# Performance work log

Hardware: AMD Instinct MI355X
Metric: run time of the kernel (lower is better)

## Reference

```python
import jax, jax.numpy as jnp
import numpy as np

# NOTE on reconstructed deps (not shown in source):
#  - utils.mmnorm(x): max-magnitude norm, x / (max|x| over last dim + eps)
#  - model.LearnableFourierResampler(din, dout, nf): x -> Linear(din,nf) -> [sin,cos] -> Linear(2nf,dout)
#  - utils.pscan(q, fn, identity): Hillis-Steele log-depth scan: for n in 1,2,4,...:
#        q = fn(x=q, y=shift_right(q, n, fill=identity))   (Scanner.forward(x, y) cats (y, x))

B, T, C, NF = 8, 2048, 1024, 64
EPS = 1e-6

def mmnorm(x):
    return x / (jnp.max(jnp.abs(x), axis=-1, keepdims=True) + EPS)

def setup_inputs() -> dict:
    key = jax.random.key(0)
    ks = jax.random.split(key, 8)
    def w(k, shape, fan_in):
        return jax.random.normal(k, shape, jnp.float32) * (1.0 / np.sqrt(fan_in))
    return {
        "x": jax.random.normal(ks[0], (B, T, C), jnp.float32),
        "attn_W": w(ks[1], (C, 2 * C), C),
        "attn_b": jnp.zeros((2 * C,), jnp.float32),
        "freq_W": w(ks[2], (2 * C, NF), 2 * C),
        "freq_b": jnp.zeros((NF,), jnp.float32),
        "out_W": w(ks[3], (2 * NF, C), 2 * NF),
        "out_b": jnp.zeros((C,), jnp.float32),
        "proj_W": w(ks[4], (C, C), C),
        "proj_b": jnp.zeros((C,), jnp.float32),
        "identity": jax.random.uniform(ks[5], (C,), jnp.float32),
    }

def _scanner(y, x, freq_W, freq_b, out_W, out_b):
    # Scanner.forward(x, y): z = cat((y, x)); Fourier resample; mmnorm
    z = jnp.concatenate([y, x], axis=-1)                      # [B,T,2C]
    f = z @ freq_W + freq_b                                   # [B,T,NF]
    z = jnp.concatenate([jnp.sin(f), jnp.cos(f)], -1) @ out_W + out_b  # [B,T,C]
    return mmnorm(z)

def reference(x, attn_W, attn_b, freq_W, freq_b, out_W, out_b, proj_W, proj_b, identity):
    b, t, c = x.shape
    qv = x @ attn_W + attn_b
    q, v = qv[..., :c], qv[..., c:]
    # Hillis-Steele parallel scan with nonlinear learned combine
    n = 1
    while n < t:
        prev = jnp.concatenate(
            [jnp.broadcast_to(identity, (b, n, c)), q[:, : t - n]], axis=1)
        q = _scanner(prev, q, freq_W, freq_b, out_W, out_b)
        n *= 2
    Y = q * v
    return Y @ proj_W + proj_b
```

## Files before the change

### kernel.cpp

```cpp
#include <hip/hip_runtime.h>
#include <hip/hip_bf16.h>
#include <math.h>


#define R_ROWS 16384
#define T_DIM  2048
#define C_DIM  1024

typedef unsigned short u16;
typedef __attribute__((ext_vector_type(8))) short short8;
typedef __attribute__((ext_vector_type(4))) float f32x4;

__device__ __forceinline__ u16 f2bf(float f) {
  union { float f; unsigned u; } v; v.f = f;
  unsigned r = v.u + 0x7fffu + ((v.u >> 16) & 1u);
  return (u16)(r >> 16);
}
__device__ __forceinline__ float bf2f(u16 h) {
  union { unsigned u; float f; } v; v.u = ((unsigned)h) << 16;
  return v.f;
}
__device__ __forceinline__ void gld16(const void* g, void* l) {
  __builtin_amdgcn_global_load_lds(
      (const __attribute__((address_space(1))) void*)g,
      (__attribute__((address_space(3))) void*)l, 16, 0, 0);
}

__global__ __launch_bounds__(256) void cvt_bf16(const float* __restrict__ in,
                                                u16* __restrict__ out, int n8) {
  const int i = blockIdx.x * 256 + threadIdx.x;
  if (i >= n8) return;
  const float4 a = ((const float4*)in)[2 * i];
  const float4 b = ((const float4*)in)[2 * i + 1];
  alignas(16) u16 t[8] = {f2bf(a.x), f2bf(a.y), f2bf(a.z), f2bf(a.w),
                          f2bf(b.x), f2bf(b.y), f2bf(b.z), f2bf(b.w)};
  ((uint4*)out)[i] = *(const uint4*)t;
}

__device__ __forceinline__ void cvtT_tile(const float* W, u16* Wt, int K, int N,
                                          int noff, int k0, int n0,
                                          float (*t)[33]) {
  const int tx = threadIdx.x & 31, ty = threadIdx.x >> 5;
#pragma unroll
  for (int i = 0; i < 32; i += 8)
    t[ty + i][tx] = W[(size_t)(k0 + ty + i) * N + noff + n0 + tx];
  __syncthreads();
#pragma unroll
  for (int i = 0; i < 32; i += 8)
    Wt[(size_t)(n0 + ty + i) * K + k0 + tx] = f2bf(t[tx][ty + i]);
}

__global__ __launch_bounds__(256) void prep_weights(
    const float* __restrict__ attn_W, const float* __restrict__ proj_W,
    const float* __restrict__ out_W, const float* __restrict__ freq_W,
    u16* __restrict__ aWt, u16* __restrict__ pWt, u16* __restrict__ w2t,
    u16* __restrict__ w1f, u16* __restrict__ Wqb, u16* __restrict__ Wob) {
  __shared__ float t[32][33];
  const int bid = blockIdx.x;
  if (bid < 1024) {
    cvtT_tile(attn_W, aWt, 1024, 2048, 1024, (bid & 31) * 32, (bid >> 5) * 32, t);
  } else if (bid < 2048) {
    const int b = bid - 1024;
    cvtT_tile(proj_W, pWt, 1024, 1024, 0, (b & 31) * 32, (b >> 5) * 32, t);
  } else if (bid < 2176) {
    const int b = bid - 2048;
    cvtT_tile(out_W, w2t, 128, 1024, 0, (b & 3) * 32, (b >> 2) * 32, t);
  } else if (bid < 2304) {
    const int b = bid - 2176;
    const int k0 = (b & 63) * 32, n0 = (b >> 6) * 32;
    const int tx = threadIdx.x & 31, ty = threadIdx.x >> 5;
#pragma unroll
    for (int i = 0; i < 32; i += 8)
      t[ty + i][tx] = freq_W[(size_t)(k0 + ty + i) * 64 + n0 + tx];
    __syncthreads();
#pragma unroll
    for (int i = 0; i < 32; i += 8) {
      const int k = k0 + tx;
      const int row = (n0 + ty + i) + ((k >= 1024) ? 64 : 0);
      w1f[(size_t)row * 1024 + (k & 1023)] = f2bf(t[tx][ty + i]);
    }
  } else if (bid < 3328) {
    const int c = bid - 2304, k0 = threadIdx.x * 4;
    const float4 a = *(const float4*)&attn_W[(size_t)c * 2048 + k0];
    alignas(8) u16 tt[4] = {f2bf(a.x), f2bf(a.y), f2bf(a.z), f2bf(a.w)};
    *(uint2*)&Wqb[(size_t)c * 1024 + k0] = *(const uint2*)tt;
  } else {
    const int c = bid - 3328, k0 = threadIdx.x * 4;
    const float4 a = *(const float4*)&out_W[(size_t)c * 1024 + k0];
    alignas(8) u16 tt[4] = {f2bf(a.x), f2bf(a.y), f2bf(a.z), f2bf(a.w)};
    *(uint2*)&Wob[(size_t)c * 1024 + k0] = *(const uint2*)tt;
  }
}

__device__ __forceinline__ void gm_body(const u16* w1f, const u16* B,
                                        u16* Mt, int ldO, int n0, u16* As) {
  const int tid = threadIdx.x, lane = tid & 63, w = tid >> 6;
  const int ln = lane & 15, qd = lane >> 4;
  const int wm = w & 1, wn = w >> 1;
  const int srow = w * 32 + (lane >> 3);
  const int scol = ((lane & 7) ^ ((lane >> 3) & 7)) * 8;
  f32x4 acc[4][2] = {};
  for (int kt = 0; kt < 1024; kt += 64) {
    __syncthreads();
#pragma unroll
    for (int j = 0; j < 4; j++)
      gld16(&w1f[(size_t)(srow + j * 8) * 1024 + kt + scol],
            &As[(w * 32 + j * 8) * 64]);
    __syncthreads();
#pragma unroll
    for (int ks = 0; ks < 2; ks++) {
      short8 af[4];
#pragma unroll
      for (int i = 0; i < 4; i++) {
        const int ar = wm * 64 + i * 16 + ln;
        af[i] = *(const short8*)&As[ar * 64 + ((ks * 4 + qd) ^ (ar & 7)) * 8];
      }
#pragma unroll
      for (int nt = 0; nt < 2; nt++) {
        const short8 b = *(const short8*)&B[(size_t)(n0 + wn * 32 + nt * 16 + ln) * 1024 +
                                            kt + ks * 32 + qd * 8];
#pragma unroll
        for (int i = 0; i < 4; i++)
          acc[i][nt] = __builtin_amdgcn_mfma_f32_16x16x32_bf16(af[i], b, acc[i][nt], 0, 0, 0);
      }
    }
  }
#pragma unroll
  for (int i = 0; i < 4; i++)
#pragma unroll
    for (int nt = 0; nt < 2; nt++)
#pragma unroll
      for (int r = 0; r < 4; r++)
        Mt[(size_t)(wm * 64 + i * 16 + qd * 4 + r) * ldO +
           n0 + wn * 32 + nt * 16 + ln] = f2bf(acc[i][nt][r]);
}

__device__ __forceinline__ void dotred_body(const float* ab, const u16* w1f,
                                            float* outv, float* red) {
  const int tid = threadIdx.x, j = tid >> 1, part = tid & 1;
  float s = 0.f;
  for (int k = part * 512; k < part * 512 + 512; k++)
    s += ab[k] * bf2f(w1f[(size_t)j * 1024 + k]);
  red[tid] = s;
  __syncthreads();
  if (part == 0) outv[j] = red[2 * j] + red[2 * j + 1];
}

__global__ __launch_bounds__(256) void prep_small(
    const float* __restrict__ ident, const float* __restrict__ freq_W,
    const float* __restrict__ attn_b, const float* __restrict__ out_b,
    const u16* __restrict__ w1f, const u16* __restrict__ Wqb,
    const u16* __restrict__ Wob, float* __restrict__ fid,
    float* __restrict__ bgv, float* __restrict__ c1,
    u16* __restrict__ Mt, u16* __restrict__ W21t) {
  __shared__ u16 sh[8192];
  float* red = (float*)sh;
  const int bid = blockIdx.x;
  if (bid == 0) {
    const int tid = threadIdx.x;
    const int j = tid >> 2, part = tid & 3;
    float s = 0.f;
    for (int k = part * 256; k < part * 256 + 256; k++)
      s += ident[k] * freq_W[(size_t)k * 64 + j];
    red[tid] = s;
    __syncthreads();
    if (part == 0) fid[j] = red[tid] + red[tid + 1] + red[tid + 2] + red[tid + 3];
  } else if (bid == 1) {
    dotred_body(attn_b, w1f, bgv, red);
  } else if (bid == 2) {
    dotred_body(out_b, w1f, c1, red);
  } else if (bid < 19) {
    gm_body(w1f, Wqb, Mt, 1024, (bid - 3) * 64, sh);
  } else {
    gm_body(w1f, Wob, W21t, 128, (bid - 19) * 64, sh);
  }
}

#define GEMM_KLOOP(Aptr, Bptr)                                                 \
  const int tid = threadIdx.x, lane = tid & 63, w = tid >> 6;                  \
  const int ln = lane & 15, qd = lane >> 4;                                    \
  const int wm = w & 1, wn = w >> 1;                                           \
  const int nbx = gridDim.x;                                                   \
  const int bid0 = blockIdx.y * nbx + blockIdx.x;                              \
  const int nwg = nbx * gridDim.y;                                             \
  const int bid = (bid0 & 7) * (nwg >> 3) + (bid0 >> 3);                       \
  const int n0 = (bid % nbx) * 128, m0 = (bid / nbx) * 128;                    \
  const int srow = w * 32 + (lane >> 3);                                       \
  const int sl = (lane & 7) ^ ((lane >> 3) & 7);                               \
  const int scol = sl * 8;                                                     \
  f32x4 acc[4][4] = {};                                                        \
  for (int kt = 0; kt < 1024; kt += 64) {                                      \
    __syncthreads();                                                           \
    _Pragma("unroll") for (int j = 0; j < 4; j++) {                            \
      gld16(&Aptr[(size_t)(m0 + srow + j * 8) * 1024 + kt + scol],             \
            &As[(w * 32 + j * 8) * 64]);                                       \
      gld16(&Bptr[(size_t)(n0 + srow + j * 8) * 1024 + kt + scol],             \
            &Bs[(w * 32 + j * 8) * 64]);                                       \
    }                                                                          \
    __syncthreads();                                                           \
    _Pragma("unroll") for (int ks = 0; ks < 2; ks++) {                         \
      short8 af[4], bf_[4];                                                    \
      _Pragma("unroll") for (int i = 0; i < 4; i++) {                          \
        const int ar = wm * 64 + i * 16 + ln;                                  \
        af[i] = *(const short8*)&As[ar * 64 + ((ks * 4 + qd) ^ (ar & 7)) * 8]; \
      }                                                                        \
      _Pragma("unroll") for (int j = 0; j < 4; j++) {                          \
        const int br = wn * 64 + j * 16 + ln;                                  \
        bf_[j] = *(const short8*)&Bs[br * 64 + ((ks * 4 + qd) ^ (br & 7)) * 8];\
      }                                                                        \
      _Pragma("unroll") for (int i = 0; i < 4; i++)                            \
      _Pragma("unroll") for (int j = 0; j < 4; j++)                            \
        acc[i][j] = __builtin_amdgcn_mfma_f32_16x16x32_bf16(af[i], bf_[j],     \
                                                            acc[i][j], 0, 0, 0);\
    }                                                                          \
  }                                                                            \
  __syncthreads();

__global__ __launch_bounds__(256) void gemm_v_mfma(
    const u16* __restrict__ A, const u16* __restrict__ Bt,
    const float* __restrict__ bias, u16* __restrict__ Vb) {
  __shared__ u16 S[16384];
  u16* As = S;
  u16* Bs = S + 8192;
  GEMM_KLOOP(A, Bt)
#pragma unroll
  for (int j = 0; j < 4; j++) {
    const int col = wn * 64 + j * 16 + ln;
    const float bv = bias[n0 + col];
#pragma unroll
    for (int i = 0; i < 4; i++)
#pragma unroll
      for (int r = 0; r < 4; r++)
        S[(wm * 64 + i * 16 + qd * 4 + r) * 128 + col] = f2bf(acc[i][j][r] + bv);
  }
  __syncthreads();
#pragma unroll
  for (int it = 0; it < 8; it++) {
    const int idx = it * 256 + tid;
    const int row = idx >> 4, seg = idx & 15;
    *(uint4*)&Vb[(size_t)(m0 + row) * 1024 + n0 + seg * 8] = ((const uint4*)S)[idx];
  }
}

__global__ __launch_bounds__(256) void gemm_proj_mfma(
    const u16* __restrict__ A, const u16* __restrict__ Bt,
    const float* __restrict__ bias, float* __restrict__ OUT) {
  __shared__ u16 S[16384];
  u16* As = S;
  u16* Bs = S + 8192;
  GEMM_KLOOP(A, Bt)
  float* Csf = (float*)S;
#pragma unroll
  for (int p = 0; p < 2; p++) {
    if (wm == p) {
#pragma unroll
      for (int j = 0; j < 4; j++) {
        const int col = wn * 64 + j * 16 + ln;
        const float bv = bias[n0 + col];
#pragma unroll
        for (int i = 0; i < 4; i++)
#pragma unroll
          for (int r = 0; r < 4; r++)
            Csf[(i * 16 + qd * 4 + r) * 128 + col] = acc[i][j][r] + bv;
      }
    }
    __syncthreads();
#pragma unroll
    for (int it = 0; it < 8; it++) {
      const int idx = it * 256 + tid;
      const int row = idx >> 5, seg = idx & 31;
      *(uint4*)&OUT[(size_t)(m0 + p * 64 + row) * 1024 + n0 + seg * 4] =
          ((const uint4*)Csf)[idx];
    }
    __syncthreads();
  }
}

__global__ __launch_bounds__(256) void g0_kernel(const u16* __restrict__ Xb,
                                                 const u16* __restrict__ Mt,
                                                 const float* __restrict__ bg,
                                                 float* __restrict__ G) {
  __shared__ u16 As[64 * 64];
  const int tid = threadIdx.x, lane = tid & 63, wv = tid >> 6;
  const int ln = lane & 15, qd = lane >> 4;
  const int wm = wv >> 1, wn = wv & 1;
  const int m0 = blockIdx.x * 64;
  const int srow = wv * 16 + (lane >> 3);
  const int scol = ((lane & 7) ^ ((lane >> 3) & 7)) * 8;
  f32x4 acc[2][4] = {};
  for (int kt = 0; kt < 1024; kt += 64) {
    __syncthreads();
#pragma unroll
    for (int j = 0; j < 2; j++)
      gld16(&Xb[(size_t)(m0 + srow + j * 8) * 1024 + kt + scol],
            &As[(wv * 16 + j * 8) * 64]);
    __syncthreads();
#pragma unroll
    for (int ks = 0; ks < 2; ks++) {
      short8 a[2];
#pragma unroll
      for (int i = 0; i < 2; i++) {
        const int ar = wm * 32 + i * 16 + ln;
        a[i] = *(const short8*)&As[ar * 64 + ((ks * 4 + qd) ^ (ar & 7)) * 8];
      }
#pragma unroll
      for (int nt = 0; nt < 4; nt++) {
        const short8 b = *(const short8*)&Mt[(size_t)(wn * 64 + nt * 16 + ln) * 1024 +
                                             kt + ks * 32 + qd * 8];
#pragma unroll
        for (int i = 0; i < 2; i++)
          acc[i][nt] = __builtin_amdgcn_mfma_f32_16x16x32_bf16(a[i], b, acc[i][nt], 0, 0, 0);
      }
    }
  }
#pragma unroll
  for (int i = 0; i < 2; i++)
#pragma unroll
    for (int nt = 0; nt < 4; nt++) {
      const float bgv = bg[wn * 64 + nt * 16 + ln];
#pragma unroll
      for (int r = 0; r < 4; r++)
        G[(size_t)(m0 + wm * 32 + i * 16 + qd * 4 + r) * 128 + wn * 64 + nt * 16 + ln] =
            acc[i][nt][r] + bgv;
    }
}

__global__ __launch_bounds__(1024, 4) void scan_fused(
    const float* __restrict__ Gsrc, float* __restrict__ Gdst,
    const u16* __restrict__ W21t, const u16* __restrict__ W2t,
    const float* __restrict__ b1, const float* __restrict__ b2,
    const float* __restrict__ fid, const float* __restrict__ c1,
    const u16* __restrict__ Vb, u16* __restrict__ Yout, int n, int flags) {
  __shared__ u16 S[64 * 128];
  __shared__ unsigned rmax[64];
  const int tid = threadIdx.x, lane = tid & 63, wv = tid >> 6;
  const int ln = lane & 15, qd = lane >> 4;
  const int r0 = blockIdx.x * 64;
  if (tid < 64) rmax[tid] = 0u;
  {
    const int r = tid >> 4, js = (tid & 15) << 2;
    const int gr = r0 + r, tl = gr & (T_DIM - 1);
    const float* g1p = (tl >= n) ? &Gsrc[(size_t)(gr - n) * 128 + js] : &fid[js];
    const float4 g1 = *(const float4*)g1p;
    const float4 g2 = *(const float4*)&Gsrc[(size_t)gr * 128 + 64 + js];
    const float4 bb = *(const float4*)&b1[js];
    float f[4] = {g1.x + g2.x + bb.x, g1.y + g2.y + bb.y,
                  g1.z + g2.z + bb.z, g1.w + g2.w + bb.w};
    alignas(8) u16 sn[4], cs[4];
#pragma unroll
    for (int c = 0; c < 4; c++) {
      float sv, cv;
      __sincosf(f[c], &sv, &cv);
      sn[c] = f2bf(sv);
      cs[c] = f2bf(cv);
    }
    const int u = js >> 3, half = (js >> 2) & 1, rx = r & 7;
    const int ps = (u ^ rx) & 7;
    const int pc = 8 | ps;
    *(uint2*)&S[r * 128 + ps * 8 + half * 4] = *(const uint2*)sn;
    *(uint2*)&S[r * 128 + pc * 8 + half * 4] = *(const uint2*)cs;
  }
  __syncthreads();
  const u16* w2b = W2t + (size_t)wv * 64 * 128;
  f32x4 acc[4][4] = {};
#pragma unroll
  for (int ks = 0; ks < 4; ks++) {
    short8 af[4];
#pragma unroll
    for (int i = 0; i < 4; i++) {
      const int ar = i * 16 + ln;
      const int u = ks * 4 + qd;
      af[i] = *(const short8*)&S[ar * 128 + ((u & 8) | ((u ^ ar) & 7)) * 8];
    }
#pragma unroll
    for (int nt = 0; nt < 4; nt++) {
      const short8 b = *(const short8*)&w2b[(size_t)(nt * 16 + ln) * 128 + ks * 32 + qd * 8];
#pragma unroll
      for (int i = 0; i < 4; i++)
        acc[i][nt] = __builtin_amdgcn_mfma_f32_16x16x32_bf16(b, af[i], acc[i][nt], 0, 0, 0);
    }
  }
  float mx[4] = {0.f, 0.f, 0.f, 0.f};
#pragma unroll
  for (int nt = 0; nt < 4; nt++) {
    const float4 bb = *(const float4*)&b2[wv * 64 + nt * 16 + qd * 4];
    const float br4[4] = {bb.x, bb.y, bb.z, bb.w};
#pragma unroll
    for (int i = 0; i < 4; i++)
#pragma unroll
      for (int r = 0; r < 4; r++) {
        const float v = acc[i][nt][r] + br4[r];
        acc[i][nt][r] = v;
        mx[i] = fmaxf(mx[i], fabsf(v));
      }
  }
#pragma unroll
  for (int i = 0; i < 4; i++) {
    float v = mx[i];
    v = fmaxf(v, __shfl_xor(v, 16, 64));
    v = fmaxf(v, __shfl_xor(v, 32, 64));
    if (lane < 16) atomicMax(&rmax[i * 16 + lane], __float_as_uint(v));
  }
  __syncthreads();
  if (flags & 1) {
    float inv[4];
#pragma unroll
    for (int i = 0; i < 4; i++)
      inv[i] = 1.0f / (__uint_as_float(rmax[i * 16 + ln]) + 1e-6f);
#pragma unroll
    for (int i = 0; i < 4; i++) {
      const int row = i * 16 + ln;
#pragma unroll
      for (int nt = 0; nt < 4; nt++) {
        const int col = wv * 64 + nt * 16 + qd * 4;
        const uint2 vv = *(const uint2*)&Vb[(size_t)(r0 + row) * 1024 + col];
        const u16* vp = (const u16*)&vv;
        uint2 pv;
        pv.x = (unsigned)f2bf(acc[i][nt][0] * inv[i] * bf2f(vp[0])) |
               ((unsigned)f2bf(acc[i][nt][1] * inv[i] * bf2f(vp[1])) << 16);
        pv.y = (unsigned)f2bf(acc[i][nt][2] * inv[i] * bf2f(vp[2])) |
               ((unsigned)f2bf(acc[i][nt][3] * inv[i] * bf2f(vp[3])) << 16);
        *(uint2*)&Yout[(size_t)(r0 + row) * 1024 + col] = pv;
      }
    }
  }
  if (flags & 2) {
    const int wm3 = wv & 3, wn3 = wv >> 2;
    f32x4 g[2] = {};
#pragma unroll
    for (int ks = 0; ks < 4; ks++) {
      const int ar = wm3 * 16 + ln;
      const int u = ks * 4 + qd;
      const short8 a = *(const short8*)&S[ar * 128 + ((u & 8) | ((u ^ ar) & 7)) * 8];
#pragma unroll
      for (int c = 0; c < 2; c++) {
        const short8 b = *(const short8*)&W21t[(size_t)(wn3 * 32 + c * 16 + ln) * 128 +
                                               ks * 32 + qd * 8];
        g[c] = __builtin_amdgcn_mfma_f32_16x16x32_bf16(a, b, g[c], 0, 0, 0);
      }
    }
#pragma unroll
    for (int c = 0; c < 2; c++) {
      const int col = wn3 * 32 + c * 16 + ln;
      const float cb = c1[col];
#pragma unroll
      for (int r = 0; r < 4; r++) {
        const int row = wm3 * 16 + qd * 4 + r;
        const float invr = 1.0f / (__uint_as_float(rmax[row]) + 1e-6f);
        Gdst[(size_t)(r0 + row) * 128 + col] = (g[c][r] + cb) * invr;
      }
    }
  }
}

extern "C" void kernel_launch(void* const* d_in, const int* in_sizes, int n_in,
                              void* d_out, int out_size, void* d_ws, size_t ws_size,
                              hipStream_t stream) {
  const float* x      = (const float*)d_in[0];
  const float* attn_W = (const float*)d_in[1];
  const float* attn_b = (const float*)d_in[2];
  const float* freq_W = (const float*)d_in[3];
  const float* freq_b = (const float*)d_in[4];
  const float* out_W  = (const float*)d_in[5];
  const float* out_b  = (const float*)d_in[6];
  const float* proj_W = (const float*)d_in[7];
  const float* proj_b = (const float*)d_in[8];
  const float* ident  = (const float*)d_in[9];
  float* out = (float*)d_out;

  const size_t RC = (size_t)R_ROWS * C_DIM;
  u16* Xb  = (u16*)d_ws;
  u16* Qb  = Xb + RC;
  u16* Wqb = Qb;
  u16* Mt  = Qb + (size_t)1024 * 1024;
  u16* Wob = Mt + (size_t)128 * 1024;
  u16* Vb  = Qb + RC;
  u16* aWt = Vb + RC;
  u16* pWt = aWt + (size_t)2048 * 1024;
  u16* w2t = pWt + (size_t)1024 * 1024;
  u16* w1f = w2t + (size_t)1024 * 128;
  float* Ga  = (float*)(w1f + (size_t)128 * 1024);
  float* Gb  = Ga + (size_t)R_ROWS * 128;
  float* fid = Gb + (size_t)R_ROWS * 128;
  float* c1  = fid + 64;
  float* bgv = c1 + 128;
  u16* W21t  = (u16*)(bgv + 128);

  cvt_bf16<<<8192, 256, 0, stream>>>(x, Xb, (int)(RC / 8));
  prep_weights<<<3456, 256, 0, stream>>>(attn_W, proj_W, out_W, freq_W,
                                         aWt, pWt, w2t, w1f, Wqb, Wob);
  prep_small<<<21, 256, 0, stream>>>(ident, freq_W, attn_b, out_b, w1f, Wqb,
                                     Wob, fid, bgv, c1, Mt, W21t);

  gemm_v_mfma<<<dim3(8, 128), 256, 0, stream>>>(Xb, aWt, attn_b + 1024, Vb);
  g0_kernel<<<256, 256, 0, stream>>>(Xb, Mt, bgv, Ga);

  float* gs = Ga;
  float* gd = Gb;
  for (int n = 1; n < 1024; n <<= 1) {
    scan_fused<<<256, 1024, 0, stream>>>(gs, gd, W21t, w2t, freq_b, out_b, fid,
                                         c1, Vb, Xb, n, 2);
    float* t = gs; gs = gd; gd = t;
  }
  scan_fused<<<256, 1024, 0, stream>>>(gs, gd, W21t, w2t, freq_b, out_b, fid,
                                       c1, Vb, Xb, 1024, 1);

  gemm_proj_mfma<<<dim3(8, 128), 256, 0, stream>>>(Xb, pWt, proj_b, out);
}
```

Measured before the change: 373.9 us.

## Fuse initial G projection into V GEMM and swizzle scan block order

```diff
diff --git a/kernel.cpp b/kernel.cpp
--- a/kernel.cpp
+++ b/kernel.cpp
@@ -216,29 +216,44 @@
   }                                                                            \
   __syncthreads();
 
-__global__ __launch_bounds__(256) void gemm_v_mfma(
+__global__ __launch_bounds__(256) void gemm_vg_mfma(
     const u16* __restrict__ A, const u16* __restrict__ Bt,
-    const float* __restrict__ bias, u16* __restrict__ Vb) {
+    const float* __restrict__ bias, const float* __restrict__ bg,
+    u16* __restrict__ Vb, float* __restrict__ G) {
   __shared__ u16 S[16384];
   u16* As = S;
   u16* Bs = S + 8192;
   GEMM_KLOOP(A, Bt)
-#pragma unroll
-  for (int j = 0; j < 4; j++) {
-    const int col = wn * 64 + j * 16 + ln;
-    const float bv = bias[n0 + col];
-#pragma unroll
-    for (int i = 0; i < 4; i++)
-#pragma unroll
-      for (int r = 0; r < 4; r++)
-        S[(wm * 64 + i * 16 + qd * 4 + r) * 128 + col] = f2bf(acc[i][j][r] + bv);
-  }
-  __syncthreads();
-#pragma unroll
-  for (int it = 0; it < 8; it++) {
-    const int idx = it * 256 + tid;
-    const int row = idx >> 4, seg = idx & 15;
-    *(uint4*)&Vb[(size_t)(m0 + row) * 1024 + n0 + seg * 8] = ((const uint4*)S)[idx];
+  if (n0 < 1024) {
+#pragma unroll
+    for (int j = 0; j < 4; j++) {
+      const int col = wn * 64 + j * 16 + ln;
+      const float bv = bias[n0 + col];
+#pragma unroll
+      for (int i = 0; i < 4; i++)
+#pragma unroll
+        for (int r = 0; r < 4; r++)
+          S[(wm * 64 + i * 16 + qd * 4 + r) * 128 + col] = f2bf(acc[i][j][r] + bv);
+    }
+    __syncthreads();
+#pragma unroll
+    for (int it = 0; it < 8; it++) {
+      const int idx = it * 256 + tid;
+      const int row = idx >> 4, seg = idx & 15;
+      *(uint4*)&Vb[(size_t)(m0 + row) * 1024 + n0 + seg * 8] = ((const uint4*)S)[idx];
+    }
+  } else {
+#pragma unroll
+    for (int j = 0; j < 4; j++) {
+      const int col = wn * 64 + j * 16 + ln;
+      const float bv = bg[col];
+#pragma unroll
+      for (int i = 0; i < 4; i++)
+#pragma unroll
+        for (int r = 0; r < 4; r++)
+          G[(size_t)(m0 + wm * 64 + i * 16 + qd * 4 + r) * 128 + col] =
+              acc[i][j][r] + bv;
+    }
   }
 }
 
@@ -274,55 +289,6 @@
     }
     __syncthreads();
   }
-}
-
-__global__ __launch_bounds__(256) void g0_kernel(const u16* __restrict__ Xb,
-                                                 const u16* __restrict__ Mt,
-                                                 const float* __restrict__ bg,
-                                                 float* __restrict__ G) {
-  __shared__ u16 As[64 * 64];
-  const int tid = threadIdx.x, lane = tid & 63, wv = tid >> 6;
-  const int ln = lane & 15, qd = lane >> 4;
-  const int wm = wv >> 1, wn = wv & 1;
-  const int m0 = blockIdx.x * 64;
-  const int srow = wv * 16 + (lane >> 3);
-  const int scol = ((lane & 7) ^ ((lane >> 3) & 7)) * 8;
-  f32x4 acc[2][4] = {};
-  for (int kt = 0; kt < 1024; kt += 64) {
-    __syncthreads();
-#pragma unroll
-    for (int j = 0; j < 2; j++)
-      gld16(&Xb[(size_t)(m0 + srow + j * 8) * 1024 + kt + scol],
-            &As[(wv * 16 + j * 8) * 64]);
-    __syncthreads();
-#pragma unroll
-    for (int ks = 0; ks < 2; ks++) {
-      short8 a[2];
-#pragma unroll
-      for (int i = 0; i < 2; i++) {
-        const int ar = wm * 32 + i * 16 + ln;
-        a[i] = *(const short8*)&As[ar * 64 + ((ks * 4 + qd) ^ (ar & 7)) * 8];
-      }
-#pragma unroll
-      for (int nt = 0; nt < 4; nt++) {
-        const short8 b = *(const short8*)&Mt[(size_t)(wn * 64 + nt * 16 + ln) * 1024 +
-                                             kt + ks * 32 + qd * 8];
-#pragma unroll
-        for (int i = 0; i < 2; i++)
-          acc[i][nt] = __builtin_amdgcn_mfma_f32_16x16x32_bf16(a[i], b, acc[i][nt], 0, 0, 0);
-      }
-    }
-  }
-#pragma unroll
-  for (int i = 0; i < 2; i++)
-#pragma unroll
-    for (int nt = 0; nt < 4; nt++) {
-      const float bgv = bg[wn * 64 + nt * 16 + ln];
-#pragma unroll
-      for (int r = 0; r < 4; r++)
-        G[(size_t)(m0 + wm * 32 + i * 16 + qd * 4 + r) * 128 + wn * 64 + nt * 16 + ln] =
-            acc[i][nt][r] + bgv;
-    }
 }
 
 __global__ __launch_bounds__(1024, 4) void scan_fused(
@@ -335,7 +301,8 @@
   __shared__ unsigned rmax[64];
   const int tid = threadIdx.x, lane = tid & 63, wv = tid >> 6;
   const int ln = lane & 15, qd = lane >> 4;
-  const int r0 = blockIdx.x * 64;
+  const int bid = blockIdx.x;
+  const int r0 = (((bid & 7) << 5) + (bid >> 3)) * 64;
   if (tid < 64) rmax[tid] = 0u;
   {
     const int r = tid >> 4, js = (tid & 15) << 2;
@@ -472,10 +439,10 @@
   u16* Xb  = (u16*)d_ws;
   u16* Qb  = Xb + RC;
   u16* Wqb = Qb;
-  u16* Mt  = Qb + (size_t)1024 * 1024;
-  u16* Wob = Mt + (size_t)128 * 1024;
+  u16* Wob = Qb + (size_t)1024 * 1024;
   u16* Vb  = Qb + RC;
   u16* aWt = Vb + RC;
+  u16* Mt  = aWt + (size_t)1024 * 1024;
   u16* pWt = aWt + (size_t)2048 * 1024;
   u16* w2t = pWt + (size_t)1024 * 1024;
   u16* w1f = w2t + (size_t)1024 * 128;
@@ -492,8 +459,8 @@
   prep_small<<<21, 256, 0, stream>>>(ident, freq_W, attn_b, out_b, w1f, Wqb,
                                      Wob, fid, bgv, c1, Mt, W21t);
 
-  gemm_v_mfma<<<dim3(8, 128), 256, 0, stream>>>(Xb, aWt, attn_b + 1024, Vb);
-  g0_kernel<<<256, 256, 0, stream>>>(Xb, Mt, bgv, Ga);
+  gemm_vg_mfma<<<dim3(9, 128), 256, 0, stream>>>(Xb, aWt, attn_b + 1024, bgv,
+                                                 Vb, Ga);
 
   float* gs = Ga;
   float* gd = Gb;
```

Result: faster. 359.4 us (-3.9%).
